# Kernel optimization log

Hardware: AMD Instinct MI355X
Metric: run time of the kernel (lower is better)

Reference implementation:

```python
import jax, jax.numpy as jnp
import numpy as np

DIM = 256
NUM_HEADS = 8
HEAD_DIM = DIM // NUM_HEADS
SCALE = HEAD_DIM ** (-0.5)


def setup_inputs() -> dict:
    key = jax.random.key(0)
    k1, k2, k3, k4 = jax.random.split(key, 4)
    x = jax.random.normal(k1, (4, 1, DIM, 12, 12, 12), dtype=jnp.float32)
    w_qkv = jax.random.normal(k2, (3 * DIM, DIM), dtype=jnp.float32) * 0.02
    w_proj = jax.random.normal(k3, (DIM, DIM), dtype=jnp.float32) * 0.02
    b_proj = jax.random.normal(k4, (DIM,), dtype=jnp.float32) * 0.02
    return {"x": x, "w_qkv": w_qkv, "w_proj": w_proj, "b_proj": b_proj}


def reference(x, w_qkv, w_proj, b_proj):
    # x: [P=4, B, C, H, W, D]; 1x1x1 Conv3d == channel matmul
    P, B, C, H, W, D = x.shape
    N = H * W * D
    xf = x.reshape(P, B, C, N)                       # [P,B,C,N]
    qkv = jnp.einsum('pbcn,oc->pbon', xf, w_qkv)     # [P,B,3C,N]
    q, k, v = jnp.split(qkv, 3, axis=2)              # each [P,B,C,N]
    # fold batch*heads
    def heads(t):
        return t.reshape(P, B * NUM_HEADS, HEAD_DIM, N)
    q, k, v = heads(q) * SCALE, heads(k), heads(v)
    attn = jnp.einsum('phcm,phcn->phmn', q, k)       # [P,BH,N,N]
    attn = jax.nn.softmax(attn, axis=-1)
    out = jnp.einsum('phmn,phcn->phcm', attn, v)     # [P,BH,hd,N]
    out = out.reshape(P, B, C, N)
    out = jnp.einsum('pbcn,oc->pbon', out, w_proj) + b_proj[None, None, :, None]
    return out.reshape(P, B, C, H, W, D)
```

## Files before the change

### kernel.cpp

```cpp
#include <hip/hip_runtime.h>

#define NP 4
#define NH 8
#define HD 32
#define CD 256
#define NN 1728
#define NT_TILES 27
#define TILE_E 2048
#define SCALE_Q2 (0.17677669529663687f * 1.4426950408889634f)

typedef __bf16 bf16x8 __attribute__((ext_vector_type(8)));
typedef __bf16 bf16x4_t __attribute__((ext_vector_type(4)));
typedef short short4_t __attribute__((ext_vector_type(4)));
typedef float f32x4 __attribute__((ext_vector_type(4)));
typedef unsigned short ushort4_t __attribute__((ext_vector_type(4)));
typedef unsigned short ushort8_t __attribute__((ext_vector_type(8)));

__device__ __forceinline__ float bf2f(unsigned short u) {
  unsigned int v = ((unsigned int)u) << 16;
  return __builtin_bit_cast(float, v);
}
__device__ __forceinline__ unsigned short f2bf(float f) {
  unsigned int v = __builtin_bit_cast(unsigned int, f);
  unsigned int r = (v + 0x7FFFu + ((v >> 16) & 1u)) >> 16;
  return (unsigned short)r;
}

__global__ void k_prep(const float* __restrict__ x, unsigned short* __restrict__ xt,
                       const float* __restrict__ wqkv, const float* __restrict__ wproj,
                       unsigned short* __restrict__ wq_b, unsigned short* __restrict__ wp_b) {
  __shared__ __attribute__((aligned(16))) unsigned short tile[64 * 40];
  int bid = blockIdx.x;
  int t = threadIdx.x;
  if (bid >= 864) {
    int idx = ((bid - 864) * 256 + t) * 4;
    const float* src;
    unsigned short* dst;
    if (idx < 196608) { src = wqkv + idx; dst = wq_b + idx; }
    else { src = wproj + (idx - 196608); dst = wp_b + (idx - 196608); }
    float4 v = *(const float4*)src;
    ushort4_t o;
    o[0] = f2bf(v.x); o[1] = f2bf(v.y); o[2] = f2bf(v.z); o[3] = f2bf(v.w);
    *(ushort4_t*)dst = o;
    return;
  }
  int nb = (bid % 27) * 64, cb = ((bid / 27) & 7) * 32, p = bid / 216;
  {
    int c = t >> 3, ch = t & 7;
    const float* src = x + ((size_t)p * CD + cb + c) * NN + nb + ch * 8;
    float4 v0 = *(const float4*)src;
    float4 v1 = *(const float4*)(src + 4);
    int base = ch * 8;
    tile[(base + 0) * 40 + c] = f2bf(v0.x);
    tile[(base + 1) * 40 + c] = f2bf(v0.y);
    tile[(base + 2) * 40 + c] = f2bf(v0.z);
    tile[(base + 3) * 40 + c] = f2bf(v0.w);
    tile[(base + 4) * 40 + c] = f2bf(v1.x);
    tile[(base + 5) * 40 + c] = f2bf(v1.y);
    tile[(base + 6) * 40 + c] = f2bf(v1.z);
    tile[(base + 7) * 40 + c] = f2bf(v1.w);
  }
  __syncthreads();
  {
    int n = t >> 2, ch = t & 3;
    *(ushort8_t*)(xt + ((size_t)p * NN + nb + n) * CD + cb + ch * 8) =
        *(const ushort8_t*)&tile[n * 40 + ch * 8];
  }
}

__global__ __launch_bounds__(256) void k_qkv(const unsigned short* __restrict__ xt,
                                             const unsigned short* __restrict__ wqkv,
                                             unsigned short* __restrict__ Qt,
                                             unsigned short* __restrict__ Kt,
                                             unsigned short* __restrict__ Vv) {
  __shared__ __attribute__((aligned(16))) unsigned short smem[64 * 72];
  int p = blockIdx.z, ot = blockIdx.y, nt = blockIdx.x;
  int tid = threadIdx.x, w = tid >> 6, lane = tid & 63, l15 = lane & 15, g = lane >> 4;
  int nbase = nt * 64 + w * 16;
  f32x4 acc[4] = {};
  const unsigned short* arow = xt + ((size_t)p * NN + nbase + l15) * CD + g * 8;
  const unsigned short* wrow = wqkv + ((size_t)(ot * 64 + l15)) * CD + g * 8;
  for (int ks = 0; ks < 8; ks++) {
    bf16x8 a = *(const bf16x8*)(arow + ks * 32);
#pragma unroll
    for (int ob = 0; ob < 4; ob++) {
      bf16x8 b = *(const bf16x8*)(wrow + ob * 16 * CD + ks * 32);
      acc[ob] = __builtin_amdgcn_mfma_f32_16x16x32_bf16(a, b, acc[ob], 0, 0, 0);
    }
  }
  int wq = ot >> 2;
  if (wq == 2) {
#pragma unroll
    for (int ob = 0; ob < 4; ob++) {
      int o = ot * 64 + ob * 16 + l15;
      int rem = o & 255, h = rem >> 5, cc = rem & 31;
      size_t tb = (size_t)(p * NH + h) * (NT_TILES * TILE_E) + nt * TILE_E;
      ushort4_t vs;
      for (int r = 0; r < 4; r++) vs[r] = f2bf(acc[ob][r]);
      *(ushort4_t*)(Vv + tb + (w * 2 + (cc >> 4)) * 256 + (g * 16 + (cc & 15)) * 4) = vs;
    }
    return;
  }
  float sc = (wq == 0) ? SCALE_Q2 : 1.0f;
#pragma unroll
  for (int ob = 0; ob < 4; ob++)
    for (int r = 0; r < 4; r++)
      smem[(w * 16 + g * 4 + r) * 72 + ob * 16 + l15] = f2bf(acc[ob][r] * sc);
  __syncthreads();
#pragma unroll
  for (int i = 0; i < 2; i++) {
    int cid = i * 256 + tid;
    int row = cid >> 3, oc8 = cid & 7;
    ushort8_t vv = *(const ushort8_t*)&smem[row * 72 + oc8 * 8];
    int n = nt * 64 + row;
    if (wq == 0) {
      int h = ot * 2 + (oc8 >> 2), cc8 = (oc8 & 3) * 8;
      *(ushort8_t*)(Qt + ((size_t)(p * NH + h) * NN + n) * HD + cc8) = vv;
    } else {
      int h = (ot - 4) * 2 + (oc8 >> 2), cc8 = (oc8 & 3) * 8;
      size_t tb = (size_t)(p * NH + h) * (NT_TILES * TILE_E) + nt * TILE_E;
      *(ushort8_t*)(Kt + tb + (row >> 4) * 512 + ((cc8 >> 3) * 16 + (row & 15)) * 8) = vv;
    }
  }
}

__global__ __launch_bounds__(256) void k_attn(const unsigned short* __restrict__ Qt,
                                              const unsigned short* __restrict__ Kt,
                                              const unsigned short* __restrict__ Vv,
                                              unsigned short* __restrict__ op0,
                                              unsigned short* __restrict__ op1,
                                              float* __restrict__ Lp) {
  __shared__ __attribute__((aligned(16))) unsigned char lds[2 * 16384];
  int tid = threadIdx.x, w = tid >> 6, lane = tid & 63, l15 = lane & 15, g = lane >> 4;
  int mt = blockIdx.x, ph = blockIdx.y, z = blockIdx.z;
  int tA = z * 14;
  int nPair = z ? 6 : 7;
  bool tail = (z == 1);
  bf16x8 qfrag = *(const bf16x8*)(Qt + ((size_t)ph * NN + mt * 64 + w * 16 + l15) * HD + g * 8);
  const unsigned short* ktb = Kt + (size_t)ph * (NT_TILES * TILE_E);
  const unsigned short* vbg = Vv + (size_t)ph * (NT_TILES * TILE_E);
  f32x4 lsum = {0.f, 0.f, 0.f, 0.f};
  f32x4 oacc[2] = {};
  f32x4 zacc = {0.f, 0.f, 0.f, 0.f};
  const int so = tid * 16;
  *(ushort8_t*)(lds + so)         = *(const ushort8_t*)(ktb + tA * TILE_E + tid * 8);
  *(ushort8_t*)(lds + 4096 + so)  = *(const ushort8_t*)(ktb + (tA + 1) * TILE_E + tid * 8);
  *(ushort8_t*)(lds + 8192 + so)  = *(const ushort8_t*)(vbg + tA * TILE_E + tid * 8);
  *(ushort8_t*)(lds + 12288 + so) = *(const ushort8_t*)(vbg + (tA + 1) * TILE_E + tid * 8);
  __syncthreads();
  auto compute = [&](const unsigned char* kb, const unsigned char* vb) {
    f32x4 s[4];
#pragma unroll
    for (int nf = 0; nf < 4; nf++) {
      bf16x8 kbv = *(const bf16x8*)(kb + nf * 1024 + lane * 16);
      s[nf] = __builtin_amdgcn_mfma_f32_16x16x32_bf16(kbv, qfrag, zacc, 0, 0, 0);
    }
    short4_t pa[4];
#pragma unroll
    for (int nf = 0; nf < 4; nf++) {
      f32x4 e;
#pragma unroll
      for (int r = 0; r < 4; r++) e[r] = __builtin_amdgcn_exp2f(s[nf][r]);
      lsum += e;
      bf16x4_t t;
#pragma unroll
      for (int r = 0; r < 4; r++) t[r] = (__bf16)e[r];
      pa[nf] = __builtin_bit_cast(short4_t, t);
    }
#pragma unroll
    for (int nf = 0; nf < 4; nf++) {
#pragma unroll
      for (int cb = 0; cb < 2; cb++) {
        ushort4_t vq = *(const ushort4_t*)(vb + (nf * 2 + cb) * 512 + lane * 8);
        short4_t va = __builtin_bit_cast(short4_t, vq);
        oacc[cb] = __builtin_amdgcn_mfma_f32_16x16x16bf16_1k(va, pa[nf], oacc[cb], 0, 0, 0);
      }
    }
  };
  for (int pr = 0; pr < nPair; pr++) {
    unsigned char* buf = lds + (pr & 1) * 16384;
    unsigned char* bufN = lds + ((pr + 1) & 1) * 16384;
    ushort8_t kr0, kr1, vr0, vr1;
    bool pre = (pr + 1 < nPair);
    bool preT = tail && (pr + 1 == nPair);
    if (pre) {
      int d = tA + 2 * (pr + 1);
      kr0 = *(const ushort8_t*)(ktb + d * TILE_E + tid * 8);
      kr1 = *(const ushort8_t*)(ktb + (d + 1) * TILE_E + tid * 8);
      vr0 = *(const ushort8_t*)(vbg + d * TILE_E + tid * 8);
      vr1 = *(const ushort8_t*)(vbg + (d + 1) * TILE_E + tid * 8);
    } else if (preT) {
      kr0 = *(const ushort8_t*)(ktb + 26 * TILE_E + tid * 8);
      vr0 = *(const ushort8_t*)(vbg + 26 * TILE_E + tid * 8);
    }
    compute(buf, buf + 8192);
    compute(buf + 4096, buf + 12288);
    if (pre) {
      *(ushort8_t*)(bufN + so) = kr0;
      *(ushort8_t*)(bufN + 4096 + so) = kr1;
      *(ushort8_t*)(bufN + 8192 + so) = vr0;
      *(ushort8_t*)(bufN + 12288 + so) = vr1;
    } else if (preT) {
      *(ushort8_t*)(bufN + so) = kr0;
      *(ushort8_t*)(bufN + 8192 + so) = vr0;
    }
    __syncthreads();
  }
  if (tail) {
    unsigned char* buf = lds + (nPair & 1) * 16384;
    compute(buf, buf + 8192);
  }
  float total = lsum[0] + lsum[1] + lsum[2] + lsum[3];
  total += __shfl_xor(total, 16);
  total += __shfl_xor(total, 32);
  int m = mt * 64 + w * 16 + l15;
  unsigned short* op = z ? op1 : op0;
  if (g == 0) Lp[(size_t)z * 32 * NN + (size_t)ph * NN + m] = total;
#pragma unroll
  for (int cb = 0; cb < 2; cb++) {
    ushort4_t vs;
#pragma unroll
    for (int rr = 0; rr < 4; rr++) vs[rr] = f2bf(oacc[cb][rr]);
    *(ushort4_t*)(op + ((size_t)ph * NN + m) * 32 + cb * 16 + g * 4) = vs;
  }
}

__global__ __launch_bounds__(256) void k_proj(const unsigned short* __restrict__ op0,
                                              const unsigned short* __restrict__ op1,
                                              const float* __restrict__ Lp,
                                              const unsigned short* __restrict__ wproj,
                                              const float* __restrict__ bproj,
                                              float* __restrict__ out) {
  int p = blockIdx.z, ot = blockIdx.y, nt = blockIdx.x;
  int tid = threadIdx.x, w = tid >> 6, lane = tid & 63, l15 = lane & 15, g = lane >> 4;
  int nbase = nt * 64 + w * 16;
  int n = nbase + l15;
  f32x4 acc[4] = {};
  const unsigned short* wrow = wproj + ((size_t)(ot * 64 + l15)) * CD + g * 8;
  for (int ks = 0; ks < 8; ks++) {
    size_t r = (size_t)(p * NH + ks) * NN + n;
    float inv = 1.0f / (Lp[r] + Lp[(size_t)32 * NN + r]);
    ushort8_t a0 = *(const ushort8_t*)(op0 + r * 32 + g * 8);
    ushort8_t a1 = *(const ushort8_t*)(op1 + r * 32 + g * 8);
    bf16x8 a;
#pragma unroll
    for (int j = 0; j < 8; j++) a[j] = (__bf16)((bf2f(a0[j]) + bf2f(a1[j])) * inv);
#pragma unroll
    for (int ob = 0; ob < 4; ob++) {
      bf16x8 b = *(const bf16x8*)(wrow + ob * 16 * CD + ks * 32);
      acc[ob] = __builtin_amdgcn_mfma_f32_16x16x32_bf16(a, b, acc[ob], 0, 0, 0);
    }
  }
#pragma unroll
  for (int ob = 0; ob < 4; ob++) {
    int o = ot * 64 + ob * 16 + l15;
    float bias = bproj[o];
    int nrow = nbase + g * 4;
    float4 vs;
    vs.x = acc[ob][0] + bias;
    vs.y = acc[ob][1] + bias;
    vs.z = acc[ob][2] + bias;
    vs.w = acc[ob][3] + bias;
    *(float4*)(out + (size_t)p * CD * NN + (size_t)o * NN + nrow) = vs;
  }
}

extern "C" void kernel_launch(void* const* d_in, const int* in_sizes, int n_in,
                              void* d_out, int out_size, void* d_ws, size_t ws_size,
                              hipStream_t stream) {
  const float* x = (const float*)d_in[0];
  const float* wqkv = (const float*)d_in[1];
  const float* wproj = (const float*)d_in[2];
  const float* bproj = (const float*)d_in[3];
  float* out = (float*)d_out;
  unsigned short* ws = (unsigned short*)d_ws;
  const size_t SZ = (size_t)NP * NN * CD;
  unsigned short* xt = ws;
  unsigned short* Qt = ws + SZ;
  unsigned short* Kt = ws + 2 * SZ;
  unsigned short* Vv = ws + 3 * SZ;
  unsigned short* op1 = ws + 4 * SZ;
  unsigned short* wq_b = ws + 5 * SZ;
  unsigned short* wp_b = ws + 5 * SZ + 196608;
  float* Lp = (float*)(ws + 5 * SZ + 262144);
  unsigned short* op0 = xt;
  hipLaunchKernelGGL(k_prep, dim3(1120), dim3(256), 0, stream, x, xt, wqkv, wproj, wq_b, wp_b);
  hipLaunchKernelGGL(k_qkv, dim3(27, 12, NP), dim3(256), 0, stream, xt, wq_b, Qt, Kt, Vv);
  hipLaunchKernelGGL(k_attn, dim3(27, 32, 2), dim3(256), 0, stream, Qt, Kt, Vv, op0, op1, Lp);
  hipLaunchKernelGGL(k_proj, dim3(27, 4, NP), dim3(256), 0, stream, op0, op1, Lp, wp_b, bproj, out);
}
```

Measured before the change: 78.11 us.

## Process two query tiles per attention block to reuse K/V LDS tiles

Each attention block now handles two 64-row query tiles (128 rows) instead of one, so every K/V tile staged in LDS feeds twice as many MFMAs. The grid's x dimension shrinks from 27 to 14, and the last block handles only one tile, computing and discarding a duplicate of the first. The aim is to halve global K/V traffic and per-block staging and barrier overhead. In exchange the block count halves to 896, which lowers parallelism, and register pressure rises.

Result: slower. 80.89 us (+3.6%).

```diff
diff --git a/kernel.cpp b/kernel.cpp
--- a/kernel.cpp
+++ b/kernel.cpp
@@ -136,11 +136,16 @@
   int tA = z * 14;
   int nPair = z ? 6 : 7;
   bool tail = (z == 1);
-  bf16x8 qfrag = *(const bf16x8*)(Qt + ((size_t)ph * NN + mt * 64 + w * 16 + l15) * HD + g * 8);
+  int m1 = mt * 128 + w * 16 + l15;
+  bool valid2 = (mt < 13);
+  const unsigned short* qp1 = Qt + ((size_t)ph * NN + m1) * HD + g * 8;
+  const unsigned short* qp2 = valid2 ? (qp1 + (size_t)64 * HD) : qp1;
+  bf16x8 qf1 = *(const bf16x8*)qp1;
+  bf16x8 qf2 = *(const bf16x8*)qp2;
   const unsigned short* ktb = Kt + (size_t)ph * (NT_TILES * TILE_E);
   const unsigned short* vbg = Vv + (size_t)ph * (NT_TILES * TILE_E);
-  f32x4 lsum = {0.f, 0.f, 0.f, 0.f};
-  f32x4 oacc[2] = {};
+  f32x4 lsum1 = {0.f, 0.f, 0.f, 0.f}, lsum2 = {0.f, 0.f, 0.f, 0.f};
+  f32x4 oacc1[2] = {}, oacc2[2] = {};
   f32x4 zacc = {0.f, 0.f, 0.f, 0.f};
   const int so = tid * 16;
   *(ushort8_t*)(lds + so)         = *(const ushort8_t*)(ktb + tA * TILE_E + tid * 8);
@@ -149,23 +154,28 @@
   *(ushort8_t*)(lds + 12288 + so) = *(const ushort8_t*)(vbg + (tA + 1) * TILE_E + tid * 8);
   __syncthreads();
   auto compute = [&](const unsigned char* kb, const unsigned char* vb) {
-    f32x4 s[4];
+    f32x4 s1[4], s2[4];
 #pragma unroll
     for (int nf = 0; nf < 4; nf++) {
       bf16x8 kbv = *(const bf16x8*)(kb + nf * 1024 + lane * 16);
-      s[nf] = __builtin_amdgcn_mfma_f32_16x16x32_bf16(kbv, qfrag, zacc, 0, 0, 0);
-    }
-    short4_t pa[4];
+      s1[nf] = __builtin_amdgcn_mfma_f32_16x16x32_bf16(kbv, qf1, zacc, 0, 0, 0);
+      s2[nf] = __builtin_amdgcn_mfma_f32_16x16x32_bf16(kbv, qf2, zacc, 0, 0, 0);
+    }
+    short4_t pa1[4], pa2[4];
 #pragma unroll
     for (int nf = 0; nf < 4; nf++) {
-      f32x4 e;
-#pragma unroll
-      for (int r = 0; r < 4; r++) e[r] = __builtin_amdgcn_exp2f(s[nf][r]);
-      lsum += e;
-      bf16x4_t t;
-#pragma unroll
-      for (int r = 0; r < 4; r++) t[r] = (__bf16)e[r];
-      pa[nf] = __builtin_bit_cast(short4_t, t);
+      f32x4 e1, e2;
+#pragma unroll
+      for (int r = 0; r < 4; r++) {
+        e1[r] = __builtin_amdgcn_exp2f(s1[nf][r]);
+        e2[r] = __builtin_amdgcn_exp2f(s2[nf][r]);
+      }
+      lsum1 += e1; lsum2 += e2;
+      bf16x4_t t1, t2;
+#pragma unroll
+      for (int r = 0; r < 4; r++) { t1[r] = (__bf16)e1[r]; t2[r] = (__bf16)e2[r]; }
+      pa1[nf] = __builtin_bit_cast(short4_t, t1);
+      pa2[nf] = __builtin_bit_cast(short4_t, t2);
     }
 #pragma unroll
     for (int nf = 0; nf < 4; nf++) {
@@ -173,7 +183,8 @@
       for (int cb = 0; cb < 2; cb++) {
         ushort4_t vq = *(const ushort4_t*)(vb + (nf * 2 + cb) * 512 + lane * 8);
         short4_t va = __builtin_bit_cast(short4_t, vq);
-        oacc[cb] = __builtin_amdgcn_mfma_f32_16x16x16bf16_1k(va, pa[nf], oacc[cb], 0, 0, 0);
+        oacc1[cb] = __builtin_amdgcn_mfma_f32_16x16x16bf16_1k(va, pa1[nf], oacc1[cb], 0, 0, 0);
+        oacc2[cb] = __builtin_amdgcn_mfma_f32_16x16x16bf16_1k(va, pa2[nf], oacc2[cb], 0, 0, 0);
       }
     }
   };
@@ -210,18 +221,34 @@
     unsigned char* buf = lds + (nPair & 1) * 16384;
     compute(buf, buf + 8192);
   }
-  float total = lsum[0] + lsum[1] + lsum[2] + lsum[3];
-  total += __shfl_xor(total, 16);
-  total += __shfl_xor(total, 32);
-  int m = mt * 64 + w * 16 + l15;
   unsigned short* op = z ? op1 : op0;
-  if (g == 0) Lp[(size_t)z * 32 * NN + (size_t)ph * NN + m] = total;
-#pragma unroll
-  for (int cb = 0; cb < 2; cb++) {
-    ushort4_t vs;
-#pragma unroll
-    for (int rr = 0; rr < 4; rr++) vs[rr] = f2bf(oacc[cb][rr]);
-    *(ushort4_t*)(op + ((size_t)ph * NN + m) * 32 + cb * 16 + g * 4) = vs;
+  float* LpZ = Lp + (size_t)z * 32 * NN;
+  {
+    float total = lsum1[0] + lsum1[1] + lsum1[2] + lsum1[3];
+    total += __shfl_xor(total, 16);
+    total += __shfl_xor(total, 32);
+    if (g == 0) LpZ[(size_t)ph * NN + m1] = total;
+#pragma unroll
+    for (int cb = 0; cb < 2; cb++) {
+      ushort4_t vs;
+#pragma unroll
+      for (int rr = 0; rr < 4; rr++) vs[rr] = f2bf(oacc1[cb][rr]);
+      *(ushort4_t*)(op + ((size_t)ph * NN + m1) * 32 + cb * 16 + g * 4) = vs;
+    }
+  }
+  if (valid2) {
+    int m2 = m1 + 64;
+    float total = lsum2[0] + lsum2[1] + lsum2[2] + lsum2[3];
+    total += __shfl_xor(total, 16);
+    total += __shfl_xor(total, 32);
+    if (g == 0) LpZ[(size_t)ph * NN + m2] = total;
+#pragma unroll
+    for (int cb = 0; cb < 2; cb++) {
+      ushort4_t vs;
+#pragma unroll
+      for (int rr = 0; rr < 4; rr++) vs[rr] = f2bf(oacc2[cb][rr]);
+      *(ushort4_t*)(op + ((size_t)ph * NN + m2) * 32 + cb * 16 + g * 4) = vs;
+    }
   }
 }
 
@@ -286,6 +313,6 @@
   unsigned short* op0 = xt;
   hipLaunchKernelGGL(k_prep, dim3(1120), dim3(256), 0, stream, x, xt, wqkv, wproj, wq_b, wp_b);
   hipLaunchKernelGGL(k_qkv, dim3(27, 12, NP), dim3(256), 0, stream, xt, wq_b, Qt, Kt, Vv);
-  hipLaunchKernelGGL(k_attn, dim3(27, 32, 2), dim3(256), 0, stream, Qt, Kt, Vv, op0, op1, Lp);
+  hipLaunchKernelGGL(k_attn, dim3(14, 32, 2), dim3(256), 0, stream, Qt, Kt, Vv, op0, op1, Lp);
   hipLaunchKernelGGL(k_proj, dim3(27, 4, NP), dim3(256), 0, stream, op0, op1, Lp, wp_b, bproj, out);
 }
```

## Load V directly from global into registers and retile projection kernel

Applied to the files above, without the earlier changes.

The attention kernel no longer stages V tiles through LDS. Each thread loads its V fragments straight from global memory into registers per tile, which halves LDS use and cuts LDS traffic and stores. In exchange, the V global loads are no longer prefetched a step ahead, which may expose latency. The projection kernel moves to 128-thread blocks, each wave computing a 32x32 output tile that reuses two weight fragments across two row groups, with twice as many blocks.

Result: slower. 80.91 us (+3.6%).

```diff
diff --git a/kernel.cpp b/kernel.cpp
--- a/kernel.cpp
+++ b/kernel.cpp
@@ -130,7 +130,7 @@
                                               unsigned short* __restrict__ op0,
                                               unsigned short* __restrict__ op1,
                                               float* __restrict__ Lp) {
-  __shared__ __attribute__((aligned(16))) unsigned char lds[2 * 16384];
+  __shared__ __attribute__((aligned(16))) unsigned char lds[2 * 8192];
   int tid = threadIdx.x, w = tid >> 6, lane = tid & 63, l15 = lane & 15, g = lane >> 4;
   int mt = blockIdx.x, ph = blockIdx.y, z = blockIdx.z;
   int tA = z * 14;
@@ -143,12 +143,14 @@
   f32x4 oacc[2] = {};
   f32x4 zacc = {0.f, 0.f, 0.f, 0.f};
   const int so = tid * 16;
-  *(ushort8_t*)(lds + so)         = *(const ushort8_t*)(ktb + tA * TILE_E + tid * 8);
-  *(ushort8_t*)(lds + 4096 + so)  = *(const ushort8_t*)(ktb + (tA + 1) * TILE_E + tid * 8);
-  *(ushort8_t*)(lds + 8192 + so)  = *(const ushort8_t*)(vbg + tA * TILE_E + tid * 8);
-  *(ushort8_t*)(lds + 12288 + so) = *(const ushort8_t*)(vbg + (tA + 1) * TILE_E + tid * 8);
+  *(ushort8_t*)(lds + so)        = *(const ushort8_t*)(ktb + tA * TILE_E + tid * 8);
+  *(ushort8_t*)(lds + 4096 + so) = *(const ushort8_t*)(ktb + (tA + 1) * TILE_E + tid * 8);
   __syncthreads();
-  auto compute = [&](const unsigned char* kb, const unsigned char* vb) {
+  auto compute = [&](const unsigned char* kb, int nt) {
+    const unsigned short* vt = vbg + nt * TILE_E;
+    ushort4_t vq[8];
+#pragma unroll
+    for (int q = 0; q < 8; q++) vq[q] = *(const ushort4_t*)(vt + q * 256 + lane * 4);
     f32x4 s[4];
 #pragma unroll
     for (int nf = 0; nf < 4; nf++) {
@@ -171,44 +173,37 @@
     for (int nf = 0; nf < 4; nf++) {
 #pragma unroll
       for (int cb = 0; cb < 2; cb++) {
-        ushort4_t vq = *(const ushort4_t*)(vb + (nf * 2 + cb) * 512 + lane * 8);
-        short4_t va = __builtin_bit_cast(short4_t, vq);
+        short4_t va = __builtin_bit_cast(short4_t, vq[nf * 2 + cb]);
         oacc[cb] = __builtin_amdgcn_mfma_f32_16x16x16bf16_1k(va, pa[nf], oacc[cb], 0, 0, 0);
       }
     }
   };
   for (int pr = 0; pr < nPair; pr++) {
-    unsigned char* buf = lds + (pr & 1) * 16384;
-    unsigned char* bufN = lds + ((pr + 1) & 1) * 16384;
-    ushort8_t kr0, kr1, vr0, vr1;
+    unsigned char* buf = lds + (pr & 1) * 8192;
+    unsigned char* bufN = lds + ((pr + 1) & 1) * 8192;
+    ushort8_t kr0, kr1;
     bool pre = (pr + 1 < nPair);
     bool preT = tail && (pr + 1 == nPair);
     if (pre) {
       int d = tA + 2 * (pr + 1);
       kr0 = *(const ushort8_t*)(ktb + d * TILE_E + tid * 8);
       kr1 = *(const ushort8_t*)(ktb + (d + 1) * TILE_E + tid * 8);
-      vr0 = *(const ushort8_t*)(vbg + d * TILE_E + tid * 8);
-      vr1 = *(const ushort8_t*)(vbg + (d + 1) * TILE_E + tid * 8);
     } else if (preT) {
       kr0 = *(const ushort8_t*)(ktb + 26 * TILE_E + tid * 8);
-      vr0 = *(const ushort8_t*)(vbg + 26 * TILE_E + tid * 8);
-    }
-    compute(buf, buf + 8192);
-    compute(buf + 4096, buf + 12288);
+    }
+    compute(buf, tA + 2 * pr);
+    compute(buf + 4096, tA + 2 * pr + 1);
     if (pre) {
       *(ushort8_t*)(bufN + so) = kr0;
       *(ushort8_t*)(bufN + 4096 + so) = kr1;
-      *(ushort8_t*)(bufN + 8192 + so) = vr0;
-      *(ushort8_t*)(bufN + 12288 + so) = vr1;
     } else if (preT) {
       *(ushort8_t*)(bufN + so) = kr0;
-      *(ushort8_t*)(bufN + 8192 + so) = vr0;
     }
     __syncthreads();
   }
   if (tail) {
-    unsigned char* buf = lds + (nPair & 1) * 16384;
-    compute(buf, buf + 8192);
+    unsigned char* buf = lds + (nPair & 1) * 8192;
+    compute(buf, 26);
   }
   float total = lsum[0] + lsum[1] + lsum[2] + lsum[3];
   total += __shfl_xor(total, 16);
@@ -225,44 +220,46 @@
   }
 }
 
-__global__ __launch_bounds__(256) void k_proj(const unsigned short* __restrict__ op0,
+__global__ __launch_bounds__(128) void k_proj(const unsigned short* __restrict__ op0,
                                               const unsigned short* __restrict__ op1,
                                               const float* __restrict__ Lp,
                                               const unsigned short* __restrict__ wproj,
                                               const float* __restrict__ bproj,
                                               float* __restrict__ out) {
-  int p = blockIdx.z, ot = blockIdx.y, nt = blockIdx.x;
+  int p = blockIdx.z, oy = blockIdx.y, nt = blockIdx.x;
   int tid = threadIdx.x, w = tid >> 6, lane = tid & 63, l15 = lane & 15, g = lane >> 4;
-  int nbase = nt * 64 + w * 16;
-  int n = nbase + l15;
-  f32x4 acc[4] = {};
-  const unsigned short* wrow = wproj + ((size_t)(ot * 64 + l15)) * CD + g * 8;
+  f32x4 acc[2][2] = {};
+  const unsigned short* wrow = wproj + ((size_t)(oy * 32 + l15)) * CD + g * 8;
   for (int ks = 0; ks < 8; ks++) {
-    size_t r = (size_t)(p * NH + ks) * NN + n;
-    float inv = 1.0f / (Lp[r] + Lp[(size_t)32 * NN + r]);
-    ushort8_t a0 = *(const ushort8_t*)(op0 + r * 32 + g * 8);
-    ushort8_t a1 = *(const ushort8_t*)(op1 + r * 32 + g * 8);
-    bf16x8 a;
-#pragma unroll
-    for (int j = 0; j < 8; j++) a[j] = (__bf16)((bf2f(a0[j]) + bf2f(a1[j])) * inv);
-#pragma unroll
-    for (int ob = 0; ob < 4; ob++) {
-      bf16x8 b = *(const bf16x8*)(wrow + ob * 16 * CD + ks * 32);
-      acc[ob] = __builtin_amdgcn_mfma_f32_16x16x32_bf16(a, b, acc[ob], 0, 0, 0);
-    }
-  }
-#pragma unroll
-  for (int ob = 0; ob < 4; ob++) {
-    int o = ot * 64 + ob * 16 + l15;
-    float bias = bproj[o];
-    int nrow = nbase + g * 4;
-    float4 vs;
-    vs.x = acc[ob][0] + bias;
-    vs.y = acc[ob][1] + bias;
-    vs.z = acc[ob][2] + bias;
-    vs.w = acc[ob][3] + bias;
-    *(float4*)(out + (size_t)p * CD * NN + (size_t)o * NN + nrow) = vs;
-  }
+    bf16x8 b0 = *(const bf16x8*)(wrow + ks * 32);
+    bf16x8 b1 = *(const bf16x8*)(wrow + 16 * CD + ks * 32);
+#pragma unroll
+    for (int i = 0; i < 2; i++) {
+      int n = nt * 64 + w * 32 + i * 16 + l15;
+      size_t r = (size_t)(p * NH + ks) * NN + n;
+      float inv = 1.0f / (Lp[r] + Lp[(size_t)32 * NN + r]);
+      ushort8_t a0 = *(const ushort8_t*)(op0 + r * 32 + g * 8);
+      ushort8_t a1 = *(const ushort8_t*)(op1 + r * 32 + g * 8);
+      bf16x8 a;
+#pragma unroll
+      for (int j = 0; j < 8; j++) a[j] = (__bf16)((bf2f(a0[j]) + bf2f(a1[j])) * inv);
+      acc[i][0] = __builtin_amdgcn_mfma_f32_16x16x32_bf16(a, b0, acc[i][0], 0, 0, 0);
+      acc[i][1] = __builtin_amdgcn_mfma_f32_16x16x32_bf16(a, b1, acc[i][1], 0, 0, 0);
+    }
+  }
+#pragma unroll
+  for (int i = 0; i < 2; i++)
+    for (int ob = 0; ob < 2; ob++) {
+      int o = oy * 32 + ob * 16 + l15;
+      float bias = bproj[o];
+      int nrow = nt * 64 + w * 32 + i * 16 + g * 4;
+      float4 vs;
+      vs.x = acc[i][ob][0] + bias;
+      vs.y = acc[i][ob][1] + bias;
+      vs.z = acc[i][ob][2] + bias;
+      vs.w = acc[i][ob][3] + bias;
+      *(float4*)(out + (size_t)p * CD * NN + (size_t)o * NN + nrow) = vs;
+    }
 }
 
 extern "C" void kernel_launch(void* const* d_in, const int* in_sizes, int n_in,
@@ -287,5 +284,5 @@
   hipLaunchKernelGGL(k_prep, dim3(1120), dim3(256), 0, stream, x, xt, wqkv, wproj, wq_b, wp_b);
   hipLaunchKernelGGL(k_qkv, dim3(27, 12, NP), dim3(256), 0, stream, xt, wq_b, Qt, Kt, Vv);
   hipLaunchKernelGGL(k_attn, dim3(27, 32, 2), dim3(256), 0, stream, Qt, Kt, Vv, op0, op1, Lp);
-  hipLaunchKernelGGL(k_proj, dim3(27, 4, NP), dim3(256), 0, stream, op0, op1, Lp, wp_b, bproj, out);
-}
+  hipLaunchKernelGGL(k_proj, dim3(27, 8, NP), dim3(128), 0, stream, op0, op1, Lp, wp_b, bproj, out);
+}
```
